# Performance work log

Hardware: AMD Instinct MI355X
Metric: run time of the kernel (lower is better)

The kernel has to match this reference:

```python
import jax, jax.numpy as jnp
import numpy as np

B, N, H, E, STEPS = 16, 512, 128, 4, 5
ANNO = 1


def _edge_states(y):
    # y: [B, N, H*E] -> torch view(B,N,H,E).transpose(2,3).transpose(1,2) -> [B,E,N,H] -> [B,N*E,H]
    return y.reshape(B, N, H, E).transpose(0, 3, 1, 2).reshape(B, N * E, H)


def setup_inputs() -> dict:
    key = jax.random.key(0)
    ks = jax.random.split(key, 20)
    s = 0.05
    inp = {
        "x": jax.random.normal(ks[0], (B, N, H), jnp.float32),
        "a": jax.random.normal(ks[1], (B, N, ANNO), jnp.float32),
        "m": jax.random.uniform(ks[2], (B, N, N * E * 2), jnp.float32),
        # fc_in / fc_out: Linear(H, H*E); weights stored [in, out]
        "W_in": jax.random.normal(ks[3], (H, H * E), jnp.float32) * s,
        "b_in": jnp.zeros((H * E,), jnp.float32),
        "W_out": jax.random.normal(ks[4], (H, H * E), jnp.float32) * s,
        "b_out": jnp.zeros((H * E,), jnp.float32),
        # GatedPropagation gates: Linear(3H, H)
        "W_z": jax.random.normal(ks[5], (3 * H, H), jnp.float32) * s,
        "b_z": jnp.zeros((H,), jnp.float32),
        "W_r": jax.random.normal(ks[6], (3 * H, H), jnp.float32) * s,
        "b_r": jnp.zeros((H,), jnp.float32),
        "W_t": jax.random.normal(ks[7], (3 * H, H), jnp.float32) * s,
        "b_t": jnp.zeros((H,), jnp.float32),
        # output head: fc1(H+ANNO, H), fc2(H, 1)
        "W1": jax.random.normal(ks[8], (H + ANNO, H), jnp.float32) * s,
        "b1": jnp.zeros((H,), jnp.float32),
        "W2": jax.random.normal(ks[9], (H, 1), jnp.float32) * s,
        "b2": jnp.zeros((1,), jnp.float32),
    }
    return inp


def reference(x, a, m, W_in, b_in, W_out, b_out, W_z, b_z, W_r, b_r, W_t, b_t, W1, b1, W2, b2):
    m_in = m[:, :, : N * E]   # [B, N, N*E]
    m_out = m[:, :, N * E :]  # [B, N, N*E]
    h = x
    for _ in range(STEPS):
        in_states = _edge_states(h @ W_in + b_in)    # [B, N*E, H]
        out_states = _edge_states(h @ W_out + b_out)  # [B, N*E, H]
        a_in = jnp.einsum('bnm,bmh->bnh', m_in, in_states)
        a_out = jnp.einsum('bnm,bmh->bnh', m_out, out_states)
        cat = jnp.concatenate((a_in, a_out, h), axis=2)  # [B, N, 3H]
        z = jax.nn.sigmoid(cat @ W_z + b_z)
        r = jax.nn.sigmoid(cat @ W_r + b_r)
        joint = jnp.concatenate((a_in, a_out, r * h), axis=2)
        h_hat = jnp.tanh(joint @ W_t + b_t)
        h = (1 - z) * h + z * h_hat
    feat = jnp.tanh(jnp.concatenate((h, a), axis=2) @ W1 + b1)  # [B, N, H]
    out = (feat @ W2 + b2).sum(axis=2)  # [B, N]
    return out
```

## Files before the change

### kernel.cpp

```cpp
#include <hip/hip_runtime.h>
#include <math.h>

#define BB 16
#define NN 512
#define HH 128
#define EE 4
#define NSTEPS 5
#define ROWS (BB*NN)
#define KDIM (NN*EE)

typedef _Float16 f16x8 __attribute__((ext_vector_type(8)));
typedef float f32x4 __attribute__((ext_vector_type(4)));

#define MFMA(a,b,c) __builtin_amdgcn_mfma_f32_16x16x32_f16(a, b, c, 0, 0, 0)

__device__ inline void split8v(float4 u, float4 v, f16x8& hi, f16x8& lo) {
    float f[8] = {u.x, u.y, u.z, u.w, v.x, v.y, v.z, v.w};
    #pragma unroll
    for (int i = 0; i < 8; i++) {
        _Float16 h = (_Float16)f[i];
        hi[i] = h;
        lo[i] = (_Float16)(f[i] - (float)h);
    }
}

__device__ inline void split1(float v, _Float16* __restrict__ hp, _Float16* __restrict__ lp) {
    _Float16 h = (_Float16)v;
    *hp = h;
    *lp = (_Float16)(v - (float)h);
}

__device__ __forceinline__ void async16(void* lds, const void* g) {
    __builtin_amdgcn_global_load_lds(
        (const __attribute__((address_space(1))) void*)g,
        (__attribute__((address_space(3))) void*)lds,
        16, 0, 0);
}

__global__ void prep_kernel(const float* __restrict__ x,
                            const float* __restrict__ W_in, const float* __restrict__ b_in,
                            const float* __restrict__ W_out, const float* __restrict__ b_out,
                            const float* __restrict__ W_z, const float* __restrict__ W_r,
                            const float* __restrict__ W_t,
                            _Float16* __restrict__ WpTh, _Float16* __restrict__ WpTl,
                            float* __restrict__ bp,
                            _Float16* __restrict__ WzrtH, _Float16* __restrict__ WzrtL,
                            _Float16* __restrict__ Wt1h, _Float16* __restrict__ Wt1l,
                            _Float16* __restrict__ hHi, _Float16* __restrict__ hLo) {
    int idx = blockIdx.x * 256 + threadIdx.x;
    if (idx < 131072) {
        int c = idx >> 7, k = idx & 127;
        int io = c >> 9, cc = c & 511, e = cc >> 7, hh = cc & 127;
        const float* W = io ? W_out : W_in;
        split1(W[k * 512 + hh * 4 + e], WpTh + idx, WpTl + idx);
        if (k == 0) bp[c] = (io ? b_out : b_in)[hh * 4 + e];
    } else if (idx < 131072 + 147456) {
        int j = idx - 131072;
        int c = j / 384, k = j - c * 384;
        float v;
        if (c < 128)      v = W_z[k * 128 + c];
        else if (c < 256) v = W_r[k * 128 + (c - 128)];
        else              v = (k < 256) ? W_t[k * 128 + (c - 256)] : 0.0f;
        split1(v, WzrtH + j, WzrtL + j);
    } else if (idx < 131072 + 147456 + 16384) {
        int j = idx - 131072 - 147456;
        int c = j >> 7, k = j & 127;
        split1(W_t[(256 + k) * 128 + c], Wt1h + j, Wt1l + j);
    } else if (idx < 131072 + 147456 + 16384 + 1048576) {
        int j = idx - 131072 - 147456 - 16384;
        split1(x[j], hHi + j, hLo + j);
    }
}

__global__ __launch_bounds__(256) void xw_mfma(
        const _Float16* __restrict__ hHi, const _Float16* __restrict__ hLo,
        const _Float16* __restrict__ WpTh, const _Float16* __restrict__ WpTl,
        const float* __restrict__ bp,
        _Float16* __restrict__ YpTh, _Float16* __restrict__ YpTl) {
    const int tid = threadIdx.x;
    const int c0 = blockIdx.x * 64;
    const int n0 = blockIdx.y * 128;
    const int b  = blockIdx.z;
    const int w = tid >> 6, l = tid & 63;
    const int lm = l & 15, q = l >> 4;
    const int wr = (w & 1) * 32, wc = (w >> 1) * 64;
    f32x4 zero = {0.f, 0.f, 0.f, 0.f};
    f32x4 acc[2][4];
    #pragma unroll
    for (int i = 0; i < 2; i++)
        #pragma unroll
        for (int j = 0; j < 4; j++) acc[i][j] = zero;
    const size_t aoff = (size_t)(c0 + wr + lm) * 128 + q * 8;
    const size_t boff = (size_t)(b * 512 + n0 + wc + lm) * 128 + q * 8;
    #pragma unroll
    for (int ki = 0; ki < 4; ki++) {
        const int kc = ki * 32;
        f16x8 a0h = *(const f16x8*)(WpTh + aoff + kc);
        f16x8 a0l = *(const f16x8*)(WpTl + aoff + kc);
        f16x8 a1h = *(const f16x8*)(WpTh + aoff + 16 * 128 + kc);
        f16x8 a1l = *(const f16x8*)(WpTl + aoff + 16 * 128 + kc);
        #pragma unroll
        for (int ct = 0; ct < 4; ct++) {
            f16x8 bh = *(const f16x8*)(hHi + boff + (size_t)(ct * 16) * 128 + kc);
            f16x8 bl = *(const f16x8*)(hLo + boff + (size_t)(ct * 16) * 128 + kc);
            acc[0][ct] = MFMA(a0h, bh, acc[0][ct]);
            acc[0][ct] = MFMA(a0h, bl, acc[0][ct]);
            acc[0][ct] = MFMA(a0l, bh, acc[0][ct]);
            acc[1][ct] = MFMA(a1h, bh, acc[1][ct]);
            acc[1][ct] = MFMA(a1h, bl, acc[1][ct]);
            acc[1][ct] = MFMA(a1l, bh, acc[1][ct]);
        }
    }
    #pragma unroll
    for (int rg = 0; rg < 2; rg++)
        #pragma unroll
        for (int rr = 0; rr < 4; rr++) {
            int c = c0 + wr + rg * 16 + q * 4 + rr;
            float bias = bp[c];
            size_t d = ((size_t)b * 1024 + c) * 512 + n0 + wc + lm;
            #pragma unroll
            for (int ct = 0; ct < 4; ct++) {
                float v = acc[rg][ct][rr] + bias;
                split1(v, YpTh + d + ct * 16, YpTl + d + ct * 16);
            }
        }
}

__global__ __launch_bounds__(256) void msg_mfma(const float* __restrict__ m,
        const _Float16* __restrict__ YpTh, const _Float16* __restrict__ YpTl,
        float* __restrict__ Apart) {
    __shared__ float    mlds[3][64 * 32];
    __shared__ _Float16 ylds[3][128 * 64];

    const int tid = threadIdx.x;
    const int w = tid >> 6, l = tid & 63;
    const int lm = l & 15, q = l >> 4;
    const int wr = (w & 1) * 32, wc = (w >> 1) * 64;

    const int wg = blockIdx.x;
    const int xcd = wg & 7;
    const int s8  = wg >> 3;
    const int gi  = s8 >> 3;
    const int t8  = s8 & 7;
    const int g   = gi * 8 + xcd;
    const int ez  = g & 1, biz = g >> 1;
    const int b = biz >> 1, io = biz & 1;
    const int n0 = t8 * 64;

    const float*    mg  = m    + (size_t)(b * 512 + n0) * 4096 + io * 2048 + ez * 1024;
    const _Float16* yhg = YpTh + (size_t)(b * 1024 + io * 512 + ez * 256) * 512;
    const _Float16* ylg = YpTl + (size_t)(b * 1024 + io * 512 + ez * 256) * 512;

    f32x4 zero = {0.f, 0.f, 0.f, 0.f};
    f32x4 acc[2][4];
    #pragma unroll
    for (int i = 0; i < 2; i++)
        #pragma unroll
        for (int j = 0; j < 4; j++) acc[i][j] = zero;

    #define STAGE(buf, eee, kt) do {                                           \
        const size_t moff = (size_t)(eee) * 512 + (size_t)(kt) * 32;           \
        const size_t yoff = (size_t)(eee) * 65536 + (size_t)(kt) * 32;         \
        _Pragma("unroll")                                                      \
        for (int j = 0; j < 2; j++) {                   \
            int gi2 = w * 128 + j * 64 + l;                                    \
            int r = gi2 >> 3, pg = gi2 & 7;                                    \
            int lg = pg ^ (r & 7);                                             \
            async16(&mlds[buf][(w * 128 + j * 64) * 4],                        \
                    mg + (size_t)r * 4096 + moff + lg * 4);                    \
        }                                                                      \
        _Pragma("unroll")                                                      \
        for (int j = 0; j < 4; j++) {          \
            int gi2 = w * 256 + j * 64 + l;                                    \
            int r = gi2 >> 3, pg = gi2 & 7;                                    \
            int lg = pg ^ (r & 7);                                             \
            const _Float16* src = (lg < 4 ? yhg : ylg)                         \
                                  + (size_t)r * 512 + yoff + (lg & 3) * 8;     \
            async16(&ylds[buf][(w * 256 + j * 64) * 8], src);                  \
        }                                                                      \
    } while (0)

    #define COMPUTE(buf) do {                                                  \
        f16x8 ah[2], al[2];                                                    \
        _Pragma("unroll")                                                      \
        for (int rg = 0; rg < 2; rg++) {                                       \
            int r = wr + rg * 16 + lm, sw = r & 7;                             \
            const float* mrow = &mlds[buf][r * 32];                            \
            float4 u = *(const float4*)(mrow + (((2 * q) ^ sw) * 4));          \
            float4 v = *(const float4*)(mrow + (((2 * q + 1) ^ sw) * 4));      \
            split8v(u, v, ah[rg], al[rg]);                                     \
        }                                                                      \
        _Pragma("unroll")                                                      \
        for (int ct = 0; ct < 4; ct++) {                                       \
            int r = wc + ct * 16 + lm, sw = r & 7;                             \
            const _Float16* yrow = &ylds[buf][r * 64];                         \
            f16x8 bh = *(const f16x8*)(yrow + ((q ^ sw) * 8));                 \
            f16x8 bl = *(const f16x8*)(yrow + (((4 + q) ^ sw) * 8));           \
            acc[0][ct] = MFMA(ah[0], bh, acc[0][ct]);                          \
            acc[0][ct] = MFMA(ah[0], bl, acc[0][ct]);                          \
            acc[0][ct] = MFMA(al[0], bh, acc[0][ct]);                          \
            acc[1][ct] = MFMA(ah[1], bh, acc[1][ct]);                          \
            acc[1][ct] = MFMA(ah[1], bl, acc[1][ct]);                          \
            acc[1][ct] = MFMA(al[1], bh, acc[1][ct]);                          \
        }                                                                      \
    } while (0)

    STAGE(0, 0, 0);
    STAGE(1, 0, 1);
    #pragma unroll
    for (int ee = 0; ee < 2; ee++) {
        #pragma unroll
        for (int kt = 0; kt < 16; kt++) {
            const int t = ee * 16 + kt;
            if (t + 2 < 32) {
                const int t2 = t + 2;
                const int b2 = t2 - (t2 / 3) * 3;
                STAGE(b2, t2 >> 4, t2 & 15);
            }
            if (t <= 29)      asm volatile("s_waitcnt vmcnt(12)" ::: "memory");
            else if (t == 30) asm volatile("s_waitcnt vmcnt(6)"  ::: "memory");
            else              asm volatile("s_waitcnt vmcnt(0)"  ::: "memory");
            __builtin_amdgcn_s_barrier();
            __builtin_amdgcn_sched_barrier(0);
            COMPUTE(t - (t / 3) * 3);
            __builtin_amdgcn_sched_barrier(0);
            __builtin_amdgcn_s_barrier();
        }
    }
    #undef STAGE
    #undef COMPUTE

    float* Ap = Apart + (((size_t)(ez * 32 + biz) * 512) + n0 + wr) * 128 + wc;
    #pragma unroll
    for (int rg = 0; rg < 2; rg++)
        #pragma unroll
        for (int ct = 0; ct < 4; ct++)
            #pragma unroll
            for (int rr = 0; rr < 4; rr++)
                Ap[(size_t)(rg * 16 + q * 4 + rr) * 128 + ct * 16 + lm] = acc[rg][ct][rr];
}

__global__ __launch_bounds__(256) void msg_reduce(const float* __restrict__ Apart,
        _Float16* __restrict__ AinH, _Float16* __restrict__ AinL,
        _Float16* __restrict__ AoutH, _Float16* __restrict__ AoutL) {
    const size_t SL = (size_t)32 * 512 * 128;
    size_t idx = ((size_t)blockIdx.x * 256 + threadIdx.x) * 4;
    float4 v0 = *(const float4*)(Apart + idx);
    float4 v1 = *(const float4*)(Apart + idx + SL);
    float s[4] = {v0.x + v1.x, v0.y + v1.y, v0.z + v1.z, v0.w + v1.w};
    int biz = (int)(idx >> 16);
    int rem = (int)(idx & 65535);
    int b = biz >> 1, io = biz & 1;
    size_t d = ((size_t)b << 16) + rem;
    _Float16* Ah = (io ? AoutH : AinH) + d;
    _Float16* Al = (io ? AoutL : AinL) + d;
    #pragma unroll
    for (int j = 0; j < 4; j++) split1(s[j], Ah + j, Al + j);
}

__global__ __launch_bounds__(256) void gate_gemm1(
        const _Float16* __restrict__ AinH, const _Float16* __restrict__ AinL,
        const _Float16* __restrict__ AoutH, const _Float16* __restrict__ AoutL,
        const _Float16* __restrict__ hHi, const _Float16* __restrict__ hLo,
        const _Float16* __restrict__ WzrtH, const _Float16* __restrict__ WzrtL,
        const float* __restrict__ hcur, const float* __restrict__ b_r,
        float* __restrict__ ZRT,
        _Float16* __restrict__ RHh, _Float16* __restrict__ RHl) {
    const int tid = threadIdx.x;
    const int row0 = blockIdx.x * 64;
    const int c0 = blockIdx.y * 128;
    const int w = tid >> 6, l = tid & 63;
    const int lm = l & 15, q = l >> 4;
    const int wr = (w & 1) * 32, wc = (w >> 1) * 64;
    const size_t rA0 = (size_t)(row0 + wr + lm) * 128 + q * 8;
    const size_t rA1 = rA0 + 16 * 128;
    f32x4 zero = {0.f, 0.f, 0.f, 0.f};
    f32x4 acc[2][4];
    #pragma unroll
    for (int i = 0; i < 2; i++)
        #pragma unroll
        for (int j = 0; j < 4; j++) acc[i][j] = zero;
    const size_t woff = (size_t)(c0 + wc + lm) * 384 + q * 8;
    #pragma unroll
    for (int ph = 0; ph < 3; ph++) {
        const _Float16* Xh = (ph == 0) ? AinH : (ph == 1) ? AoutH : hHi;
        const _Float16* Xl = (ph == 0) ? AinL : (ph == 1) ? AoutL : hLo;
        #pragma unroll
        for (int ki = 0; ki < 4; ki++) {
            const int kc = ki * 32;
            f16x8 a0h = *(const f16x8*)(Xh + rA0 + kc);
            f16x8 a0l = *(const f16x8*)(Xl + rA0 + kc);
            f16x8 a1h = *(const f16x8*)(Xh + rA1 + kc);
            f16x8 a1l = *(const f16x8*)(Xl + rA1 + kc);
            const int kg = ph * 128 + kc;
            #pragma unroll
            for (int ct = 0; ct < 4; ct++) {
                f16x8 bh = *(const f16x8*)(WzrtH + woff + (size_t)(ct * 16) * 384 + kg);
                f16x8 bl = *(const f16x8*)(WzrtL + woff + (size_t)(ct * 16) * 384 + kg);
                acc[0][ct] = MFMA(a0h, bh, acc[0][ct]);
                acc[0][ct] = MFMA(a0h, bl, acc[0][ct]);
                acc[0][ct] = MFMA(a0l, bh, acc[0][ct]);
                acc[1][ct] = MFMA(a1h, bh, acc[1][ct]);
                acc[1][ct] = MFMA(a1h, bl, acc[1][ct]);
                acc[1][ct] = MFMA(a1l, bh, acc[1][ct]);
            }
        }
    }
    if (blockIdx.y == 1) {
        #pragma unroll
        for (int rg = 0; rg < 2; rg++)
            #pragma unroll
            for (int ct = 0; ct < 4; ct++)
                #pragma unroll
                for (int rr = 0; rr < 4; rr++) {
                    int grow = row0 + wr + rg * 16 + q * 4 + rr;
                    int col = wc + ct * 16 + lm;
                    float rp = acc[rg][ct][rr] + b_r[col];
                    float r = 1.0f / (1.0f + expf(-rp));
                    size_t d = (size_t)grow * 128 + col;
                    split1(r * hcur[d], RHh + d, RHl + d);
                }
    } else {
        #pragma unroll
        for (int rg = 0; rg < 2; rg++)
            #pragma unroll
            for (int ct = 0; ct < 4; ct++)
                #pragma unroll
                for (int rr = 0; rr < 4; rr++)
                    ZRT[(size_t)(row0 + wr + rg * 16 + q * 4 + rr) * 384 + c0 + wc + ct * 16 + lm] =
                        acc[rg][ct][rr];
    }
}

__global__ __launch_bounds__(256) void gate_gemm2(
        const _Float16* __restrict__ RHh, const _Float16* __restrict__ RHl,
        const _Float16* __restrict__ Wt1h, const _Float16* __restrict__ Wt1l,
        const float* __restrict__ ZRT, const float* __restrict__ hcur,
        const float* __restrict__ b_z, const float* __restrict__ b_t,
        float* __restrict__ hnF, _Float16* __restrict__ hnH, _Float16* __restrict__ hnL) {
    const int tid = threadIdx.x;
    const int row0 = blockIdx.x * 32;
    const int w = tid >> 6, l = tid & 63;
    const int lm = l & 15, q = l >> 4;
    const int wr = (w & 1) * 16, wc = (w >> 1) * 64;
    f32x4 zero = {0.f, 0.f, 0.f, 0.f};
    f32x4 acc[4] = {zero, zero, zero, zero};
    const size_t aoff = (size_t)(row0 + wr + lm) * 128 + q * 8;
    const size_t woff = (size_t)(wc + lm) * 128 + q * 8;
    #pragma unroll
    for (int ki = 0; ki < 4; ki++) {
        const int kc = ki * 32;
        f16x8 ah = *(const f16x8*)(RHh + aoff + kc);
        f16x8 al = *(const f16x8*)(RHl + aoff + kc);
        #pragma unroll
        for (int ct = 0; ct < 4; ct++) {
            f16x8 bh = *(const f16x8*)(Wt1h + woff + (size_t)(ct * 16) * 128 + kc);
            f16x8 bl = *(const f16x8*)(Wt1l + woff + (size_t)(ct * 16) * 128 + kc);
            acc[ct] = MFMA(ah, bh, acc[ct]);
            acc[ct] = MFMA(ah, bl, acc[ct]);
            acc[ct] = MFMA(al, bh, acc[ct]);
        }
    }
    #pragma unroll
    for (int ct = 0; ct < 4; ct++)
        #pragma unroll
        for (int rr = 0; rr < 4; rr++) {
            int grow = row0 + wr + q * 4 + rr;
            int col = wc + ct * 16 + lm;
            float tp = acc[ct][rr] + ZRT[(size_t)grow * 384 + 256 + col] + b_t[col];
            float hhat = tanhf(tp);
            float zp = ZRT[(size_t)grow * 384 + col] + b_z[col];
            float z = 1.0f / (1.0f + expf(-zp));
            float hv = hcur[(size_t)grow * 128 + col];
            float hn = (1.0f - z) * hv + z * hhat;
            size_t d = (size_t)grow * 128 + col;
            hnF[d] = hn;
            split1(hn, hnH + d, hnL + d);
        }
}

__global__ __launch_bounds__(128) void out_kernel(
        const float* __restrict__ hfin, const float* __restrict__ a,
        const float* __restrict__ W1, const float* __restrict__ b1,
        const float* __restrict__ W2, const float* __restrict__ b2,
        float* __restrict__ out) {
    __shared__ float hrow[129];
    __shared__ float red[2];
    const int tid = threadIdx.x;
    const int grow = blockIdx.x;
    hrow[tid] = hfin[(size_t)grow * HH + tid];
    if (tid == 0) hrow[128] = a[grow];
    __syncthreads();
    float acc = b1[tid];
    for (int k = 0; k < 129; k++) acc += hrow[k] * W1[k * HH + tid];
    float feat = tanhf(acc);
    float p = feat * W2[tid];
    #pragma unroll
    for (int off = 32; off > 0; off >>= 1) p += __shfl_down(p, off, 64);
    if ((tid & 63) == 0) red[tid >> 6] = p;
    __syncthreads();
    if (tid == 0) out[grow] = red[0] + red[1] + b2[0];
}

extern "C" void kernel_launch(void* const* d_in, const int* in_sizes, int n_in,
                              void* d_out, int out_size, void* d_ws, size_t ws_size,
                              hipStream_t stream) {
    const float* x    = (const float*)d_in[0];
    const float* a    = (const float*)d_in[1];
    const float* m    = (const float*)d_in[2];
    const float* W_in = (const float*)d_in[3];
    const float* b_in = (const float*)d_in[4];
    const float* W_out= (const float*)d_in[5];
    const float* b_out= (const float*)d_in[6];
    const float* W_z  = (const float*)d_in[7];
    const float* b_z  = (const float*)d_in[8];
    const float* W_r  = (const float*)d_in[9];
    const float* b_r  = (const float*)d_in[10];
    const float* W_t  = (const float*)d_in[11];
    const float* b_t  = (const float*)d_in[12];
    const float* W1   = (const float*)d_in[13];
    const float* b1   = (const float*)d_in[14];
    const float* W2   = (const float*)d_in[15];
    const float* b2   = (const float*)d_in[16];
    float* out = (float*)d_out;

    char* p = (char*)d_ws;
    _Float16* WpTh  = (_Float16*)p; p += 262144;
    _Float16* WpTl  = (_Float16*)p; p += 262144;
    float*    bp    = (float*)p;    p += 4096;
    _Float16* WzrtH = (_Float16*)p; p += 294912;
    _Float16* WzrtL = (_Float16*)p; p += 294912;
    _Float16* Wt1h  = (_Float16*)p; p += 32768;
    _Float16* Wt1l  = (_Float16*)p; p += 32768;
    _Float16* YpTh  = (_Float16*)p; p += 16777216;
    _Float16* YpTl  = (_Float16*)p; p += 16777216;
    _Float16* AinH  = (_Float16*)p; p += 2097152;
    _Float16* AinL  = (_Float16*)p; p += 2097152;
    _Float16* AoutH = (_Float16*)p; p += 2097152;
    _Float16* AoutL = (_Float16*)p; p += 2097152;
    _Float16* RHh   = (_Float16*)p; p += 2097152;
    _Float16* RHl   = (_Float16*)p; p += 2097152;
    float*    ZRT   = (float*)p;    p += 12582912;
    float*    hA    = (float*)p;    p += 4194304;
    float*    hB    = (float*)p;    p += 4194304;
    _Float16* hHiA  = (_Float16*)p; p += 2097152;
    _Float16* hLoA  = (_Float16*)p; p += 2097152;
    _Float16* hHiB  = (_Float16*)p; p += 2097152;
    _Float16* hLoB  = (_Float16*)p; p += 2097152;
    float*    Apart = (float*)p;    p += 33554432;

    prep_kernel<<<5248, 256, 0, stream>>>(x, W_in, b_in, W_out, b_out, W_z, W_r, W_t,
                                          WpTh, WpTl, bp, WzrtH, WzrtL, Wt1h, Wt1l,
                                          hHiA, hLoA);

    const float* curF = x;
    const _Float16 *curH = hHiA, *curL = hLoA;
    for (int s = 0; s < NSTEPS; s++) {
        float*    nF = (s & 1) ? hB : hA;
        _Float16* nH = (s & 1) ? hHiA : hHiB;
        _Float16* nL = (s & 1) ? hLoA : hLoB;
        xw_mfma<<<dim3(16, 4, 16), 256, 0, stream>>>(curH, curL, WpTh, WpTl, bp, YpTh, YpTl);
        msg_mfma<<<dim3(512), 256, 0, stream>>>(m, YpTh, YpTl, Apart);
        msg_reduce<<<2048, 256, 0, stream>>>(Apart, AinH, AinL, AoutH, AoutL);
        gate_gemm1<<<dim3(128, 3), 256, 0, stream>>>(AinH, AinL, AoutH, AoutL,
                                                     curH, curL, WzrtH, WzrtL,
                                                     curF, b_r, ZRT, RHh, RHl);
        gate_gemm2<<<256, 256, 0, stream>>>(RHh, RHl, Wt1h, Wt1l, ZRT, curF,
                                            b_z, b_t, nF, nH, nL);
        curF = nF; curH = nH; curL = nL;
    }
    out_kernel<<<ROWS, 128, 0, stream>>>(curF, a, W1, b1, W2, b2, out);
}
```

Measured before the change: 839.4 us.

## Load message matrix into registers, deepen Y ring, and MFMA the output head

In msg_mfma, the fp32 adjacency tiles now go straight from global memory into a three-deep register ring instead of through LDS. The f16 Y tiles use a four-slot LDS ring, which cuts each iteration to one barrier, and MFMA sections run at raised wave priority. The per-row scalar output kernel is replaced by an MFMA kernel that works on 32 rows per block, using a transposed, split-f16 copy of W1 built in the prep kernel. The gain is fewer LDS round trips and barriers in the dominant message GEMM, at the cost of more registers and less coalesced global reads of m.

```diff
diff --git a/kernel.cpp b/kernel.cpp
--- a/kernel.cpp
+++ b/kernel.cpp
@@ -41,12 +41,13 @@
                             const float* __restrict__ W_in, const float* __restrict__ b_in,
                             const float* __restrict__ W_out, const float* __restrict__ b_out,
                             const float* __restrict__ W_z, const float* __restrict__ W_r,
-                            const float* __restrict__ W_t,
+                            const float* __restrict__ W_t, const float* __restrict__ W1,
                             _Float16* __restrict__ WpTh, _Float16* __restrict__ WpTl,
                             float* __restrict__ bp,
                             _Float16* __restrict__ WzrtH, _Float16* __restrict__ WzrtL,
                             _Float16* __restrict__ Wt1h, _Float16* __restrict__ Wt1l,
-                            _Float16* __restrict__ hHi, _Float16* __restrict__ hLo) {
+                            _Float16* __restrict__ hHi, _Float16* __restrict__ hLo,
+                            _Float16* __restrict__ W1Th, _Float16* __restrict__ W1Tl) {
     int idx = blockIdx.x * 256 + threadIdx.x;
     if (idx < 131072) {
         int c = idx >> 7, k = idx & 127;
@@ -69,6 +70,10 @@
     } else if (idx < 131072 + 147456 + 16384 + 1048576) {
         int j = idx - 131072 - 147456 - 16384;
         split1(x[j], hHi + j, hLo + j);
+    } else if (idx < 131072 + 147456 + 16384 + 1048576 + 16384) {
+        int j = idx - (131072 + 147456 + 16384 + 1048576);
+        int c = j >> 7, k = j & 127;
+        split1(W1[k * 128 + c], W1Th + j, W1Tl + j);
     }
 }
 
@@ -129,8 +134,7 @@
 __global__ __launch_bounds__(256) void msg_mfma(const float* __restrict__ m,
         const _Float16* __restrict__ YpTh, const _Float16* __restrict__ YpTl,
         float* __restrict__ Apart) {
-    __shared__ float    mlds[3][64 * 32];
-    __shared__ _Float16 ylds[3][128 * 64];
+    __shared__ _Float16 ylds[4][128 * 64];
 
     const int tid = threadIdx.x;
     const int w = tid >> 6, l = tid & 63;
@@ -151,6 +155,9 @@
     const _Float16* yhg = YpTh + (size_t)(b * 1024 + io * 512 + ez * 256) * 512;
     const _Float16* ylg = YpTl + (size_t)(b * 1024 + io * 512 + ez * 256) * 512;
 
+    const float* mrow0 = mg + (size_t)(wr + lm) * 4096 + q * 8;
+    const float* mrow1 = mrow0 + (size_t)16 * 4096;
+
     f32x4 zero = {0.f, 0.f, 0.f, 0.f};
     f32x4 acc[2][4];
     #pragma unroll
@@ -158,76 +165,69 @@
         #pragma unroll
         for (int j = 0; j < 4; j++) acc[i][j] = zero;
 
-    #define STAGE(buf, eee, kt) do {                                           \
-        const size_t moff = (size_t)(eee) * 512 + (size_t)(kt) * 32;           \
-        const size_t yoff = (size_t)(eee) * 65536 + (size_t)(kt) * 32;         \
-        _Pragma("unroll")                                                      \
-        for (int j = 0; j < 2; j++) {                   \
-            int gi2 = w * 128 + j * 64 + l;                                    \
-            int r = gi2 >> 3, pg = gi2 & 7;                                    \
-            int lg = pg ^ (r & 7);                                             \
-            async16(&mlds[buf][(w * 128 + j * 64) * 4],                        \
-                    mg + (size_t)r * 4096 + moff + lg * 4);                    \
-        }                                                                      \
+    float4 mreg[3][4];
+
+    #define MLOAD(s3, eee, kt) do {                                            \
+        const size_t off = (size_t)(eee) * 512 + (size_t)(kt) * 32;            \
+        mreg[s3][0] = *(const float4*)(mrow0 + off);                           \
+        mreg[s3][1] = *(const float4*)(mrow0 + off + 4);                       \
+        mreg[s3][2] = *(const float4*)(mrow1 + off);                           \
+        mreg[s3][3] = *(const float4*)(mrow1 + off + 4);                       \
+    } while (0)
+
+    #define STAGEY(buf, eee, kt) do {                                          \
         _Pragma("unroll")                                                      \
         for (int j = 0; j < 4; j++) {          \
             int gi2 = w * 256 + j * 64 + l;                                    \
             int r = gi2 >> 3, pg = gi2 & 7;                                    \
             int lg = pg ^ (r & 7);                                             \
             const _Float16* src = (lg < 4 ? yhg : ylg)                         \
-                                  + (size_t)r * 512 + yoff + (lg & 3) * 8;     \
+                + (size_t)r * 512 + (size_t)(eee) * 65536 + (size_t)(kt) * 32  \
+                + (lg & 3) * 8;                                                \
             async16(&ylds[buf][(w * 256 + j * 64) * 8], src);                  \
         }                                                                      \
     } while (0)
 
-    #define COMPUTE(buf) do {                                                  \
-        f16x8 ah[2], al[2];                                                    \
-        _Pragma("unroll")                                                      \
-        for (int rg = 0; rg < 2; rg++) {                                       \
-            int r = wr + rg * 16 + lm, sw = r & 7;                             \
-            const float* mrow = &mlds[buf][r * 32];                            \
-            float4 u = *(const float4*)(mrow + (((2 * q) ^ sw) * 4));          \
-            float4 v = *(const float4*)(mrow + (((2 * q + 1) ^ sw) * 4));      \
-            split8v(u, v, ah[rg], al[rg]);                                     \
-        }                                                                      \
+    #define COMPUTE(buf, s3) do {                                              \
+        f16x8 ah0, al0, ah1, al1;                                              \
+        split8v(mreg[s3][0], mreg[s3][1], ah0, al0);                           \
+        split8v(mreg[s3][2], mreg[s3][3], ah1, al1);                           \
+        __builtin_amdgcn_s_setprio(1);                                         \
         _Pragma("unroll")                                                      \
         for (int ct = 0; ct < 4; ct++) {                                       \
             int r = wc + ct * 16 + lm, sw = r & 7;                             \
             const _Float16* yrow = &ylds[buf][r * 64];                         \
             f16x8 bh = *(const f16x8*)(yrow + ((q ^ sw) * 8));                 \
             f16x8 bl = *(const f16x8*)(yrow + (((4 + q) ^ sw) * 8));           \
-            acc[0][ct] = MFMA(ah[0], bh, acc[0][ct]);                          \
-            acc[0][ct] = MFMA(ah[0], bl, acc[0][ct]);                          \
-            acc[0][ct] = MFMA(al[0], bh, acc[0][ct]);                          \
-            acc[1][ct] = MFMA(ah[1], bh, acc[1][ct]);                          \
-            acc[1][ct] = MFMA(ah[1], bl, acc[1][ct]);                          \
-            acc[1][ct] = MFMA(al[1], bh, acc[1][ct]);                          \
+            acc[0][ct] = MFMA(ah0, bh, acc[0][ct]);                            \
+            acc[0][ct] = MFMA(ah0, bl, acc[0][ct]);                            \
+            acc[0][ct] = MFMA(al0, bh, acc[0][ct]);                            \
+            acc[1][ct] = MFMA(ah1, bh, acc[1][ct]);                            \
+            acc[1][ct] = MFMA(ah1, bl, acc[1][ct]);                            \
+            acc[1][ct] = MFMA(al1, bh, acc[1][ct]);                            \
         }                                                                      \
+        __builtin_amdgcn_s_setprio(0);                                         \
     } while (0)
 
-    STAGE(0, 0, 0);
-    STAGE(1, 0, 1);
-    #pragma unroll
-    for (int ee = 0; ee < 2; ee++) {
-        #pragma unroll
-        for (int kt = 0; kt < 16; kt++) {
-            const int t = ee * 16 + kt;
-            if (t + 2 < 32) {
-                const int t2 = t + 2;
-                const int b2 = t2 - (t2 / 3) * 3;
-                STAGE(b2, t2 >> 4, t2 & 15);
-            }
-            if (t <= 29)      asm volatile("s_waitcnt vmcnt(12)" ::: "memory");
-            else if (t == 30) asm volatile("s_waitcnt vmcnt(6)"  ::: "memory");
-            else              asm volatile("s_waitcnt vmcnt(0)"  ::: "memory");
-            __builtin_amdgcn_s_barrier();
-            __builtin_amdgcn_sched_barrier(0);
-            COMPUTE(t - (t / 3) * 3);
-            __builtin_amdgcn_sched_barrier(0);
-            __builtin_amdgcn_s_barrier();
-        }
-    }
-    #undef STAGE
+    MLOAD(0, 0, 0); STAGEY(0, 0, 0);
+    MLOAD(1, 0, 1); STAGEY(1, 0, 1);
+    #pragma unroll
+    for (int t = 0; t < 32; t++) {
+        if (t < 31) asm volatile("s_waitcnt vmcnt(8)" ::: "memory");
+        else        asm volatile("s_waitcnt vmcnt(0)" ::: "memory");
+        __builtin_amdgcn_s_barrier();
+        __builtin_amdgcn_sched_barrier(0);
+        if (t + 2 < 32) {
+            const int t2 = t + 2;
+            MLOAD(t2 % 3, t2 >> 4, t2 & 15);
+            STAGEY(t2 & 3, t2 >> 4, t2 & 15);
+        }
+        __builtin_amdgcn_sched_barrier(0);
+        COMPUTE(t & 3, t % 3);
+        __builtin_amdgcn_sched_barrier(0);
+    }
+    #undef MLOAD
+    #undef STAGEY
     #undef COMPUTE
 
     float* Ap = Apart + (((size_t)(ez * 32 + biz) * 512) + n0 + wr) * 128 + wc;
@@ -379,27 +379,65 @@
         }
 }
 
-__global__ __launch_bounds__(128) void out_kernel(
-        const float* __restrict__ hfin, const float* __restrict__ a,
-        const float* __restrict__ W1, const float* __restrict__ b1,
-        const float* __restrict__ W2, const float* __restrict__ b2,
-        float* __restrict__ out) {
-    __shared__ float hrow[129];
-    __shared__ float red[2];
+__global__ __launch_bounds__(256) void out_mfma(
+        const _Float16* __restrict__ hH, const _Float16* __restrict__ hL,
+        const _Float16* __restrict__ W1Th, const _Float16* __restrict__ W1Tl,
+        const float* __restrict__ W1, const float* __restrict__ a,
+        const float* __restrict__ b1, const float* __restrict__ W2,
+        const float* __restrict__ b2, float* __restrict__ out) {
+    __shared__ float red[4][16];
     const int tid = threadIdx.x;
-    const int grow = blockIdx.x;
-    hrow[tid] = hfin[(size_t)grow * HH + tid];
-    if (tid == 0) hrow[128] = a[grow];
+    const int row0 = blockIdx.x * 32;
+    const int w = tid >> 6, l = tid & 63;
+    const int lm = l & 15, q = l >> 4;
+    const int wr = (w & 1) * 16, wc = (w >> 1) * 64;
+    f32x4 zero = {0.f, 0.f, 0.f, 0.f};
+    f32x4 acc[4] = {zero, zero, zero, zero};
+    const size_t aoff = (size_t)(row0 + wr + lm) * 128 + q * 8;
+    const size_t woff = (size_t)(wc + lm) * 128 + q * 8;
+    #pragma unroll
+    for (int ki = 0; ki < 4; ki++) {
+        const int kc = ki * 32;
+        f16x8 ah = *(const f16x8*)(hH + aoff + kc);
+        f16x8 al = *(const f16x8*)(hL + aoff + kc);
+        #pragma unroll
+        for (int ct = 0; ct < 4; ct++) {
+            f16x8 bh = *(const f16x8*)(W1Th + woff + (size_t)(ct * 16) * 128 + kc);
+            f16x8 bl = *(const f16x8*)(W1Tl + woff + (size_t)(ct * 16) * 128 + kc);
+            acc[ct] = MFMA(ah, bh, acc[ct]);
+            acc[ct] = MFMA(ah, bl, acc[ct]);
+            acc[ct] = MFMA(al, bh, acc[ct]);
+        }
+    }
+    float psum[4] = {0.f, 0.f, 0.f, 0.f};
+    #pragma unroll
+    for (int ct = 0; ct < 4; ct++) {
+        int col = wc + ct * 16 + lm;
+        float w2v = W2[col];
+        float w1last = W1[128 * 128 + col];
+        float b1v = b1[col];
+        #pragma unroll
+        for (int rr = 0; rr < 4; rr++) {
+            int grow = row0 + wr + q * 4 + rr;
+            float pre = acc[ct][rr] + a[grow] * w1last + b1v;
+            psum[rr] += tanhf(pre) * w2v;
+        }
+    }
+    #pragma unroll
+    for (int rr = 0; rr < 4; rr++) {
+        float p = psum[rr];
+        p += __shfl_xor(p, 1, 64);
+        p += __shfl_xor(p, 2, 64);
+        p += __shfl_xor(p, 4, 64);
+        p += __shfl_xor(p, 8, 64);
+        if (lm == 0) red[w][q * 4 + rr] = p;
+    }
     __syncthreads();
-    float acc = b1[tid];
-    for (int k = 0; k < 129; k++) acc += hrow[k] * W1[k * HH + tid];
-    float feat = tanhf(acc);
-    float p = feat * W2[tid];
-    #pragma unroll
-    for (int off = 32; off > 0; off >>= 1) p += __shfl_down(p, off, 64);
-    if ((tid & 63) == 0) red[tid >> 6] = p;
-    __syncthreads();
-    if (tid == 0) out[grow] = red[0] + red[1] + b2[0];
+    if (tid < 32) {
+        int r = tid;
+        int wsel = (r >> 4) & 1;
+        out[row0 + r] = red[wsel][r & 15] + red[wsel + 2][r & 15] + b2[0];
+    }
 }
 
 extern "C" void kernel_launch(void* const* d_in, const int* in_sizes, int n_in,
@@ -432,6 +470,8 @@
     _Float16* WzrtL = (_Float16*)p; p += 294912;
     _Float16* Wt1h  = (_Float16*)p; p += 32768;
     _Float16* Wt1l  = (_Float16*)p; p += 32768;
+    _Float16* W1Th  = (_Float16*)p; p += 32768;
+    _Float16* W1Tl  = (_Float16*)p; p += 32768;
     _Float16* YpTh  = (_Float16*)p; p += 16777216;
     _Float16* YpTl  = (_Float16*)p; p += 16777216;
     _Float16* AinH  = (_Float16*)p; p += 2097152;
@@ -447,11 +487,11 @@
     _Float16* hLoA  = (_Float16*)p; p += 2097152;
     _Float16* hHiB  = (_Float16*)p; p += 2097152;
     _Float16* hLoB  = (_Float16*)p; p += 2097152;
-    float*    Apart = (float*)p;    p += 33554432;
-
-    prep_kernel<<<5248, 256, 0, stream>>>(x, W_in, b_in, W_out, b_out, W_z, W_r, W_t,
-                                          WpTh, WpTl, bp, WzrtH, WzrtL, Wt1h, Wt1l,
-                                          hHiA, hLoA);
+    float*    Apart = (float*)p;    p += 16777216;
+
+    prep_kernel<<<5312, 256, 0, stream>>>(x, W_in, b_in, W_out, b_out, W_z, W_r, W_t,
+                                          W1, WpTh, WpTl, bp, WzrtH, WzrtL, Wt1h, Wt1l,
+                                          hHiA, hLoA, W1Th, W1Tl);
 
     const float* curF = x;
     const _Float16 *curH = hHiA, *curL = hLoA;
@@ -469,5 +509,5 @@
                                             b_z, b_t, nF, nH, nL);
         curF = nF; curH = nH; curL = nL;
     }
-    out_kernel<<<ROWS, 128, 0, stream>>>(curF, a, W1, b1, W2, b2, out);
-}
+    out_mfma<<<256, 256, 0, stream>>>(curH, curL, W1Th, W1Tl, W1, a, b1, W2, b2, out);
+}
```

Result: slower. 886.6 us (+5.6%).
